# Kernel optimization log

Hardware: AMD Instinct MI355X
Metric: run time of the kernel (lower is better)

The kernel has to match this reference:

```python
import jax, jax.numpy as jnp
import numpy as np

D_MODEL = 2048
EXPAND = 2
D_INNER = D_MODEL * EXPAND            # 4096
HEAD_DIM = 64
NHEADS = D_INNER // HEAD_DIM          # 64
D_STATE = 128
NGROUPS = 1
D_CONV = 4
CHUNK = 256
CONV_DIM = D_INNER + 2 * NGROUPS * D_STATE      # 4352
D_IN_PROJ = 2 * D_INNER + 2 * NGROUPS * D_STATE + NHEADS  # 8512
EPS = 1e-5


def segsum(x):
    # x: [..., T] -> [..., T, T] lower-triangular segment sums (incl. diagonal)
    T = x.shape[-1]
    xc = jnp.cumsum(x, axis=-1)
    diff = xc[..., :, None] - xc[..., None, :]
    mask = jnp.tril(jnp.ones((T, T), dtype=bool))
    return jnp.where(mask, diff, -jnp.inf)


def causal_conv1d(x, w, b):
    # x: [B,L,C]  depthwise causal conv, kernel K; w: [C,K], b: [C]
    K = w.shape[1]
    L = x.shape[1]
    xp = jnp.pad(x, ((0, 0), (K - 1, 0), (0, 0)))
    y = b[None, None, :]
    for k in range(K):
        y = y + xp[:, k:k + L, :] * w[None, None, :, k]
    return jax.nn.silu(y)


def ssd_chunked(x, dt, A, B, C, Dskip):
    # x:[b,l,h,p] dt:[b,l,h] A:[h] B,C:[b,l,g,n] Dskip:[h]
    b, l, h, p = x.shape
    g, n = B.shape[2], B.shape[3]
    c = l // CHUNK
    xc = x.reshape(b, c, CHUNK, h, p)
    dtc = dt.reshape(b, c, CHUNK, h)
    Bh = jnp.repeat(B.reshape(b, c, CHUNK, g, n), h // g, axis=3)  # [b,c,s,h,n]
    Ch = jnp.repeat(C.reshape(b, c, CHUNK, g, n), h // g, axis=3)
    dA = dtc * A[None, None, None, :]            # [b,c,s,h]
    dAc = jnp.moveaxis(dA, 3, 1)                 # [b,h,c,s]
    A_cumsum = jnp.cumsum(dAc, axis=-1)          # [b,h,c,s]
    Lmat = jnp.exp(segsum(dAc))                  # [b,h,c,s,s]
    # intra-chunk (diagonal blocks)
    Y_diag = jnp.einsum('bclhn,bcshn,bhcls,bcsh,bcshp->bclhp', Ch, Bh, Lmat, dtc, xc)
    # per-chunk final states
    decay_states = jnp.exp(A_cumsum[..., -1:] - A_cumsum)   # [b,h,c,s]
    states = jnp.einsum('bclhn,bhcl,bclh,bclhp->bchpn', Bh, decay_states, dtc, xc)
    states = jnp.concatenate([jnp.zeros_like(states[:, :1]), states], axis=1)  # [b,c+1,h,p,n]
    # inter-chunk recurrence
    chunk_sums = jnp.pad(A_cumsum[..., -1], ((0, 0), (0, 0), (1, 0)))  # [b,h,c+1]
    decay_chunk = jnp.exp(segsum(chunk_sums))    # [b,h,c+1,c+1]
    new_states = jnp.einsum('bhzc,bchpn->bzhpn', decay_chunk, states)
    states_prev = new_states[:, :-1]             # state entering each chunk
    state_decay_out = jnp.exp(A_cumsum)          # [b,h,c,s]
    Y_off = jnp.einsum('bclhn,bchpn,bhcl->bclhp', Ch, states_prev, state_decay_out)
    Y = (Y_diag + Y_off).reshape(b, l, h, p) + x * Dskip[None, None, :, None]
    return Y


def gated_rmsnorm(y, z, w):
    # norm_before_gate=False: rmsnorm(y * silu(z)) * w, grouped (g=NGROUPS)
    x = y * jax.nn.silu(z)
    gs = D_INNER // NGROUPS
    xg = x.reshape(x.shape[:-1] + (NGROUPS, gs))
    var = jnp.mean(xg * xg, axis=-1, keepdims=True)
    xg = xg * jax.lax.rsqrt(var + EPS)
    return xg.reshape(x.shape) * w[None, None, :]


def setup_inputs() -> dict:
    key = jax.random.key(0)
    ks = jax.random.split(key, 9)
    B, L = 2, 2048
    return {
        'hidden_states': jax.random.normal(ks[0], (B, L, D_MODEL), jnp.float32),
        'W_in': jax.random.normal(ks[1], (D_MODEL, D_IN_PROJ), jnp.float32) * 0.02,
        'conv_w': jax.random.normal(ks[2], (CONV_DIM, D_CONV), jnp.float32) * 0.2,
        'conv_b': jax.random.normal(ks[3], (CONV_DIM,), jnp.float32) * 0.02,
        'A': -jnp.exp(jax.random.normal(ks[4], (NHEADS,), jnp.float32) * 0.5),
        'D': jax.random.normal(ks[5], (NHEADS,), jnp.float32) * 0.5,
        'dt_bias': jax.random.normal(ks[6], (NHEADS,), jnp.float32) * 0.5,
        'norm_w': jnp.ones((D_INNER,), jnp.float32) + jax.random.normal(ks[7], (D_INNER,), jnp.float32) * 0.02,
        'W_out': jax.random.normal(ks[8], (D_INNER, D_MODEL), jnp.float32) * 0.02,
    }


def reference(hidden_states, W_in, conv_w, conv_b, A, D, dt_bias, norm_w, W_out):
    b, l, _ = hidden_states.shape
    zxbcdt = hidden_states @ W_in  # [b,l,d_in_proj]
    z = zxbcdt[..., :D_INNER]
    xbc = zxbcdt[..., D_INNER:D_INNER + CONV_DIM]
    dt = zxbcdt[..., D_INNER + CONV_DIM:]
    xbc = causal_conv1d(xbc, conv_w, conv_b)
    x = xbc[..., :D_INNER].reshape(b, l, NHEADS, HEAD_DIM)
    Bs = xbc[..., D_INNER:D_INNER + NGROUPS * D_STATE].reshape(b, l, NGROUPS, D_STATE)
    Cs = xbc[..., D_INNER + NGROUPS * D_STATE:].reshape(b, l, NGROUPS, D_STATE)
    dt = jax.nn.softplus(dt + dt_bias[None, None, :])
    y = ssd_chunked(x, dt, A, Bs, Cs, D).reshape(b, l, D_INNER)
    y = gated_rmsnorm(y, z, norm_w)
    return y @ W_out
```

## Files before the change

kernel.cpp:

```cpp
#include <hip/hip_runtime.h>
#include <hip/hip_bf16.h>
#include <math.h>

#define D_MODEL   2048
#define D_INNER   4096
#define NHEADS    64
#define HEAD_DIM  64
#define D_STATE   128
#define CHUNK     256
#define CONV_DIM  (D_INNER + 2*D_STATE)
#define D_IN_PROJ (2*D_INNER + 2*D_STATE + NHEADS)
#define LD_ZX     8704
#define DT_OFF    (2*D_INNER + 2*D_STATE)
#define BATCH     2
#define SEQ       2048
#define NCHUNK    (SEQ/CHUNK)
#define EPS_RMS   1e-5f
#define MROWS     4096
#define TSTRIDE   ((size_t)MROWS * 512)

typedef unsigned short u16;
typedef __attribute__((ext_vector_type(8))) unsigned short u16x8;
typedef __attribute__((ext_vector_type(4))) unsigned short u16x4;
typedef __attribute__((ext_vector_type(8))) short bf16x8;
typedef __attribute__((ext_vector_type(4))) float f32x4;

__device__ __forceinline__ float us2f(u16 u){
    union { unsigned int i; float f; } c; c.i = ((unsigned int)u) << 16; return c.f;
}
__device__ __forceinline__ u16 f2us(float f){
    union { float f; unsigned int i; } c; c.f = f;
    unsigned int r = c.i + 0x7FFFu + ((c.i >> 16) & 1u);
    return (u16)(r >> 16);
}
__device__ __forceinline__ float siluf(float x){ return x / (1.f + expf(-x)); }

__device__ __forceinline__ void gload_lds16(const void* g, void* l) {
    __builtin_amdgcn_global_load_lds((const __attribute__((address_space(1))) void*)g,
                                     (__attribute__((address_space(3))) void*)l, 16, 0, 0);
}

#define VMCNT(n) asm volatile("s_waitcnt vmcnt(" #n ")" ::: "memory")

__device__ __forceinline__ void stage_half(const u16* __restrict__ g, size_t ldk,
                                           u16* ldsbase, int w, int lane)
{
    #pragma unroll
    for (int cc = 0; cc < 2; cc++) {
        int cb = cc * 512 + w * 64;
        int ci = cb + lane;
        int sc = ci ^ ((ci >> 3) & 7);
        gload_lds16(&g[(size_t)(sc >> 3) * ldk + (sc & 7) * 8], ldsbase + cb * 8);
    }
}

__global__ __launch_bounds__(256)
void cvt_bf16(const float* __restrict__ in, u16* __restrict__ out, int n4)
{
    int i = blockIdx.x * 256 + threadIdx.x;
    if (i >= n4) return;
    float4 v = *(const float4*)&in[(size_t)i * 4];
    u16x4 o; o[0]=f2us(v.x); o[1]=f2us(v.y); o[2]=f2us(v.z); o[3]=f2us(v.w);
    *(u16x4*)&out[(size_t)i * 4] = o;
}

__global__ __launch_bounds__(256)
void add2_bf16(float* __restrict__ out, const u16* __restrict__ t0,
               const u16* __restrict__ t1, int n8)
{
    int i = blockIdx.x * 256 + threadIdx.x;
    if (i >= n8) return;
    u16x8 a = *(const u16x8*)&t0[(size_t)i * 8];
    u16x8 b = *(const u16x8*)&t1[(size_t)i * 8];
    float* o = &out[(size_t)i * 8];
    *(float4*)&o[0] = make_float4(us2f(a[0])+us2f(b[0]), us2f(a[1])+us2f(b[1]),
                                  us2f(a[2])+us2f(b[2]), us2f(a[3])+us2f(b[3]));
    *(float4*)&o[4] = make_float4(us2f(a[4])+us2f(b[4]), us2f(a[5])+us2f(b[5]),
                                  us2f(a[6])+us2f(b[6]), us2f(a[7])+us2f(b[7]));
}

__global__ __launch_bounds__(256)
void transpose_cvt(const float* __restrict__ in, u16* __restrict__ out, int K, int N)
{
    __shared__ u16 tile[64][65];
    int k0 = blockIdx.x * 64;
    int n0 = blockIdx.y * 64;
    int t = threadIdx.x;
    #pragma unroll
    for (int q = 0; q < 16; q++) {
        int lin = q * 256 + t;
        int r = lin >> 6, c = lin & 63;
        int n = n0 + c;
        float v = (n < N) ? in[(size_t)(k0 + r) * N + n] : 0.f;
        tile[r][c] = f2us(v);
    }
    __syncthreads();
    #pragma unroll
    for (int q = 0; q < 4; q++) {
        int lin = q * 256 + t;
        int r = lin >> 4, cg = lin & 15;
        u16x4 v;
        #pragma unroll
        for (int e = 0; e < 4; e++) v[e] = tile[cg*4 + e][r];
        *(u16x4*)&out[(size_t)(n0 + r) * K + k0 + cg*4] = v;
    }
}

template<typename TC, bool KSPLIT>
__global__ __launch_bounds__(512, 1)
void gemm_8ph(const u16* __restrict__ Ag, const u16* __restrict__ Btg,
              TC* __restrict__ Cg, u16* __restrict__ Cg2,
              int M, int N, int Kext, int ldk, int ldc)
{
    __shared__ u16 smA[2][2][8192];
    __shared__ u16 smB[2][2][8192];
    const int tid = threadIdx.x;
    const int lane = tid & 63, w = tid >> 6;
    const int wm = w >> 2, wn = w & 3;
    const int lr = lane & 15, kh = lane >> 4;
    const int swz = (lr & 7) << 3;

    int orig = blockIdx.x;
    int ntile = gridDim.x;
    int kidx = 0;
    if constexpr (KSPLIT) { kidx = orig & 1; orig >>= 1; ntile >>= 1; }

    const int nbx = N >> 8;
    const int qq = ntile >> 3, r8 = ntile & 7;
    const int xcd = orig & 7, loc = orig >> 3;
    const int wgid = (xcd < r8 ? xcd*(qq+1) : r8*(qq+1) + (xcd-r8)*qq) + loc;
    const int m0 = (wgid / nbx) * 256;
    const int n0 = (wgid % nbx) * 256;

    if constexpr (KSPLIT) {
        Ag  += (size_t)kidx * Kext;
        Btg += (size_t)kidx * Kext;
        Cg2 += (size_t)kidx * M * ldc;
    }
    const int NT = Kext >> 6;

    f32x4 acc[8][4];
    #pragma unroll
    for (int i = 0; i < 8; i++)
        #pragma unroll
        for (int j = 0; j < 4; j++) acc[i][j] = (f32x4){0.f,0.f,0.f,0.f};

    stage_half(&Ag [(size_t)(m0      ) * ldk      ], ldk, &smA[0][0][0], w, lane);
    stage_half(&Ag [(size_t)(m0 + 128) * ldk      ], ldk, &smA[0][1][0], w, lane);
    stage_half(&Btg[(size_t)(n0      ) * ldk      ], ldk, &smB[0][0][0], w, lane);
    stage_half(&Btg[(size_t)(n0 + 128) * ldk      ], ldk, &smB[0][1][0], w, lane);
    stage_half(&Ag [(size_t)(m0      ) * ldk + 64 ], ldk, &smA[1][0][0], w, lane);
    stage_half(&Btg[(size_t)(n0      ) * ldk + 64 ], ldk, &smB[1][0][0], w, lane);
    stage_half(&Btg[(size_t)(n0 + 128) * ldk + 64 ], ldk, &smB[1][1][0], w, lane);
    VMCNT(6);
    __builtin_amdgcn_s_barrier();

    for (int t = 0; t < NT; ++t) {
        const int d = t & 1;
        const u16* As = &smA[d][wm][0];
        const u16* Bs = &smB[d][wn >> 1][0];
        const int rb = (wn & 1) * 64;

        bf16x8 aF[4][2], bLo[2][2], bHi[2][2];

        #pragma unroll
        for (int i = 0; i < 4; i++)
            #pragma unroll
            for (int ks = 0; ks < 2; ks++)
                aF[i][ks] = *(const bf16x8*)&As[(i*16 + lr)*64 + ((ks*32 + kh*8) ^ swz)];
        #pragma unroll
        for (int j = 0; j < 2; j++)
            #pragma unroll
            for (int ks = 0; ks < 2; ks++)
                bLo[j][ks] = *(const bf16x8*)&Bs[(rb + j*16 + lr)*64 + ((ks*32 + kh*8) ^ swz)];
        if (t + 1 < NT)
            stage_half(&Ag[(size_t)(m0 + 128) * ldk + (t+1)*64], ldk, &smA[d^1][1][0], w, lane);
        __builtin_amdgcn_s_barrier();
        __builtin_amdgcn_s_setprio(1);
        #pragma unroll
        for (int i = 0; i < 4; i++)
            #pragma unroll
            for (int j = 0; j < 2; j++)
                #pragma unroll
                for (int ks = 0; ks < 2; ks++)
                    acc[i][j] = __builtin_amdgcn_mfma_f32_16x16x32_bf16(aF[i][ks], bLo[j][ks], acc[i][j], 0, 0, 0);
        __builtin_amdgcn_s_setprio(0);
        __builtin_amdgcn_s_barrier();

        #pragma unroll
        for (int j = 0; j < 2; j++)
            #pragma unroll
            for (int ks = 0; ks < 2; ks++)
                bHi[j][ks] = *(const bf16x8*)&Bs[(rb + (2+j)*16 + lr)*64 + ((ks*32 + kh*8) ^ swz)];
        __builtin_amdgcn_s_barrier();
        __builtin_amdgcn_s_setprio(1);
        #pragma unroll
        for (int i = 0; i < 4; i++)
            #pragma unroll
            for (int j = 0; j < 2; j++)
                #pragma unroll
                for (int ks = 0; ks < 2; ks++)
                    acc[i][2+j] = __builtin_amdgcn_mfma_f32_16x16x32_bf16(aF[i][ks], bHi[j][ks], acc[i][2+j], 0, 0, 0);
        __builtin_amdgcn_s_setprio(0);
        __builtin_amdgcn_s_barrier();

        #pragma unroll
        for (int i = 0; i < 4; i++)
            #pragma unroll
            for (int ks = 0; ks < 2; ks++)
                aF[i][ks] = *(const bf16x8*)&As[(64 + i*16 + lr)*64 + ((ks*32 + kh*8) ^ swz)];
        if (t + 2 < NT)
            stage_half(&Btg[(size_t)(n0) * ldk + (t+2)*64], ldk, &smB[d][0][0], w, lane);
        __builtin_amdgcn_s_barrier();
        __builtin_amdgcn_s_setprio(1);
        #pragma unroll
        for (int i = 0; i < 4; i++)
            #pragma unroll
            for (int j = 0; j < 2; j++)
                #pragma unroll
                for (int ks = 0; ks < 2; ks++)
                    acc[4+i][j] = __builtin_amdgcn_mfma_f32_16x16x32_bf16(aF[i][ks], bLo[j][ks], acc[4+i][j], 0, 0, 0);
        __builtin_amdgcn_s_setprio(0);
        __builtin_amdgcn_s_barrier();

        if (t + 2 < NT) {
            stage_half(&Btg[(size_t)(n0 + 128) * ldk + (t+2)*64], ldk, &smB[d][1][0], w, lane);
            stage_half(&Ag [(size_t)(m0      ) * ldk + (t+2)*64], ldk, &smA[d][0][0], w, lane);
        }
        __builtin_amdgcn_s_barrier();
        __builtin_amdgcn_s_setprio(1);
        #pragma unroll
        for (int i = 0; i < 4; i++)
            #pragma unroll
            for (int j = 0; j < 2; j++)
                #pragma unroll
                for (int ks = 0; ks < 2; ks++)
                    acc[4+i][2+j] = __builtin_amdgcn_mfma_f32_16x16x32_bf16(aF[i][ks], bHi[j][ks], acc[4+i][2+j], 0, 0, 0);
        __builtin_amdgcn_s_setprio(0);
        if (t < NT - 2)       { VMCNT(6); }
        else if (t == NT - 2) { VMCNT(0); }
        __builtin_amdgcn_s_barrier();
    }

    #pragma unroll
    for (int mf = 0; mf < 8; mf++) {
        #pragma unroll
        for (int nf = 0; nf < 4; nf++) {
            int r = m0 + wm*128 + mf*16 + kh*4;
            int cidx = n0 + wn*64 + nf*16 + lr;
            #pragma unroll
            for (int q = 0; q < 4; q++) {
                if constexpr (KSPLIT) {
                    Cg2[(size_t)(r+q)*ldc + cidx] = f2us(acc[mf][nf][q]);
                } else if constexpr (sizeof(TC) == 4) {
                    Cg[(size_t)(r+q)*ldc + cidx] = acc[mf][nf][q];
                } else {
                    Cg[(size_t)(r+q)*ldc + cidx] = f2us(acc[mf][nf][q]);
                }
            }
        }
    }
}

__global__ __launch_bounds__(256)
void gemm_tail_ks4(const u16* __restrict__ A, const u16* __restrict__ Bt,
                   float* __restrict__ Cp, int M, int ldk)
{
    __shared__ u16 Asm[128][32];
    __shared__ u16 Bsm[128][32];
    const int t = threadIdx.x;
    const int lane = t & 63, w = t >> 6;
    const int wr = w >> 1, wc = w & 1;
    const int lr = lane & 15, kh = lane >> 4;

    const int bid = blockIdx.x;
    const int kidx = bid & 3, tile = bid >> 2;
    const int m0 = (tile >> 2) * 128;
    const int n0 = (tile & 3) * 128;

    const u16* Ak = A  + kidx * 512;
    const u16* Bk = Bt + kidx * 512;
    float* C = Cp + (size_t)kidx * TSTRIDE;

    f32x4 acc[4][4];
    #pragma unroll
    for (int i = 0; i < 4; i++)
        #pragma unroll
        for (int j = 0; j < 4; j++) acc[i][j] = (f32x4){0.f,0.f,0.f,0.f};

    for (int k0 = 0; k0 < 512; k0 += 32) {
        #pragma unroll
        for (int i = 0; i < 2; i++) {
            int cb = i * 256 + w * 64;
            int chunk = cb + lane;
            int row = chunk >> 2, kb = chunk & 3;
            gload_lds16(&Ak[(size_t)(m0 + row) * ldk + k0 + kb * 8], &Asm[0][0] + cb * 8);
            gload_lds16(&Bk[(size_t)(n0 + row) * ldk + k0 + kb * 8], &Bsm[0][0] + cb * 8);
        }
        __syncthreads();
        bf16x8 af[4], bf[4];
        #pragma unroll
        for (int i = 0; i < 4; i++)
            af[i] = *(const bf16x8*)&Asm[wr*64 + i*16 + lr][kh*8];
        #pragma unroll
        for (int j = 0; j < 4; j++)
            bf[j] = *(const bf16x8*)&Bsm[wc*64 + j*16 + lr][kh*8];
        #pragma unroll
        for (int i = 0; i < 4; i++)
            #pragma unroll
            for (int j = 0; j < 4; j++)
                acc[i][j] = __builtin_amdgcn_mfma_f32_16x16x32_bf16(af[i], bf[j], acc[i][j], 0, 0, 0);
        __syncthreads();
    }
    #pragma unroll
    for (int i = 0; i < 4; i++) {
        #pragma unroll
        for (int j = 0; j < 4; j++) {
            int r = m0 + wr*64 + i*16 + kh*4;
            int cidx = n0 + wc*64 + j*16 + lr;
            #pragma unroll
            for (int q = 0; q < 4; q++)
                C[(size_t)(r+q)*512 + cidx] = acc[i][j][q];
        }
    }
}

__global__ __launch_bounds__(256)
void conv_silu(const u16* __restrict__ zx, const float* __restrict__ tailp,
               const float* __restrict__ cw, const float* __restrict__ cb,
               u16* __restrict__ xconv, u16* __restrict__ Bbuf, u16* __restrict__ Cbuf)
{
    int idx = blockIdx.x * 256 + threadIdx.x;
    int cg = idx % (CONV_DIM / 8);
    int r  = idx / (CONV_DIM / 8);
    int c0 = cg * 8;
    int l  = r & (SEQ - 1);

    float y[8];
    {
        float4 b0 = *(const float4*)&cb[c0];
        float4 b1 = *(const float4*)&cb[c0 + 4];
        y[0]=b0.x; y[1]=b0.y; y[2]=b0.z; y[3]=b0.w;
        y[4]=b1.x; y[5]=b1.y; y[6]=b1.z; y[7]=b1.w;
    }
    float cwf[8][4];
    #pragma unroll
    for (int e = 0; e < 8; e++) {
        float4 v = *(const float4*)&cw[(c0 + e) * 4];
        cwf[e][0]=v.x; cwf[e][1]=v.y; cwf[e][2]=v.z; cwf[e][3]=v.w;
    }
    if (c0 < D_INNER) {
        #pragma unroll
        for (int k = 0; k < 4; k++) {
            if (l + k - 3 >= 0) {
                u16x8 v = *(const u16x8*)&zx[(size_t)(r + k - 3) * LD_ZX + D_INNER + c0];
                #pragma unroll
                for (int e = 0; e < 8; e++) y[e] += us2f(v[e]) * cwf[e][k];
            }
        }
    } else {
        int tc = c0 - D_INNER;
        #pragma unroll
        for (int k = 0; k < 4; k++) {
            if (l + k - 3 >= 0) {
                const float* tb = &tailp[(size_t)(r + k - 3) * 512 + tc];
                #pragma unroll
                for (int e = 0; e < 8; e++) {
                    float s = tb[e] + tb[TSTRIDE + e] + tb[2*TSTRIDE + e] + tb[3*TSTRIDE + e];
                    y[e] += s * cwf[e][k];
                }
            }
        }
    }
    u16x8 o;
    #pragma unroll
    for (int e = 0; e < 8; e++) {
        float s = y[e] / (1.f + expf(-y[e]));
        o[e] = f2us(s);
    }
    if (c0 < D_INNER)                *(u16x8*)&xconv[(size_t)r * D_INNER + c0] = o;
    else if (c0 < D_INNER + D_STATE) *(u16x8*)&Bbuf[(size_t)r * D_STATE + (c0 - D_INNER)] = o;
    else                             *(u16x8*)&Cbuf[(size_t)r * D_STATE + (c0 - D_INNER - D_STATE)] = o;
}

__global__ __launch_bounds__(256)
void dt_acs(const float* __restrict__ tailp, const float* __restrict__ Aparam,
            const float* __restrict__ dt_bias, float* __restrict__ dtT,
            float* __restrict__ Acs)
{
    __shared__ float sb[CHUNK];
    int blk = blockIdx.x;
    int c = blk & 7, h = (blk >> 3) & 63, b = blk >> 9;
    int t = threadIdx.x;
    int lg = c * CHUNK + t;
    int row = b * SEQ + lg;
    const float* tb = &tailp[(size_t)row * 512 + 256 + h];
    float x = tb[0] + tb[TSTRIDE] + tb[2*TSTRIDE] + tb[3*TSTRIDE];
    x += dt_bias[h];
    float dt = (x > 20.f) ? x : log1pf(expf(x));
    float v = dt * Aparam[h];
    sb[t] = v; __syncthreads();
    #pragma unroll
    for (int off = 1; off < 256; off <<= 1) {
        float add = (t >= off) ? sb[t - off] : 0.f;
        __syncthreads();
        v += add; sb[t] = v;
        __syncthreads();
    }
    int o = (b * NHEADS + h) * SEQ + lg;
    dtT[o] = dt;
    Acs[o] = v;
}

__global__ __launch_bounds__(256)
void s_precompute(const u16* __restrict__ Bbuf, const u16* __restrict__ Cbuf,
                  u16* __restrict__ Sbuf)
{
    int p = blockIdx.x % 10, bc = blockIdx.x / 10;
    int q = (p >= 6) ? 3 : (p >= 3) ? 2 : (p >= 1) ? 1 : 0;
    int st = p - q * (q + 1) / 2;
    int b = bc >> 3, c = bc & 7;
    const int lane = threadIdx.x & 63, w = threadIdx.x >> 6;
    const int lr = lane & 15, kh = lane >> 4;
    const size_t rowbase = (size_t)(b * SEQ + c * CHUNK);

    f32x4 sacc[4];
    #pragma unroll
    for (int i = 0; i < 4; i++) sacc[i] = (f32x4){0.f,0.f,0.f,0.f};
    #pragma unroll
    for (int kk = 0; kk < 4; kk++) {
        bf16x8 bA = *(const bf16x8*)&Bbuf[(rowbase + st*64 + w*16 + lr) * D_STATE + kk*32 + kh*8];
        #pragma unroll
        for (int i = 0; i < 4; i++) {
            bf16x8 af = *(const bf16x8*)&Cbuf[(rowbase + q*64 + i*16 + lr) * D_STATE + kk*32 + kh*8];
            sacc[i] = __builtin_amdgcn_mfma_f32_16x16x32_bf16(bA, af, sacc[i], 0, 0, 0);
        }
    }
    u16* Sb = Sbuf + (size_t)bc * 256 * 256;
    #pragma unroll
    for (int i = 0; i < 4; i++) {
        u16x4 o;
        #pragma unroll
        for (int qq = 0; qq < 4; qq++) o[qq] = f2us(sacc[i][qq]);
        *(u16x4*)&Sb[(size_t)(q*64 + i*16 + lr) * 256 + st*64 + w*16 + kh*4] = o;
    }
}

__global__ __launch_bounds__(256)
void chunk_states_mfma(const u16* __restrict__ xconv, const u16* __restrict__ Bbuf,
                       const float* __restrict__ dtT, const float* __restrict__ Acs,
                       u16* __restrict__ states)
{
    __shared__ u16 Btsh[128][72];
    __shared__ u16 xtsh[64][72];
    __shared__ float acs_sh[CHUNK];
    __shared__ float dt_sh[CHUNK];

    const int blk = blockIdx.x;
    const int h = blk & 63, c = (blk >> 6) & 7, b = blk >> 9;
    const int t = threadIdx.x;
    const int lane = t & 63, w = t >> 6;
    const int wr = w >> 1, wc = w & 1;
    const int lr = lane & 15, kh = lane >> 4;
    const int bh = b * NHEADS + h;
    const size_t rowbase = (size_t)(b * SEQ + c * CHUNK);

    acs_sh[t] = Acs[(size_t)bh * SEQ + c * CHUNK + t];
    dt_sh[t]  = dtT[(size_t)bh * SEQ + c * CHUNK + t];
    __syncthreads();
    const float acs_last = acs_sh[CHUNK - 1];

    f32x4 acc[4][2];
    #pragma unroll
    for (int j = 0; j < 4; j++)
        #pragma unroll
        for (int i = 0; i < 2; i++) acc[j][i] = (f32x4){0.f,0.f,0.f,0.f};

    for (int lt = 0; lt < 4; lt++) {
        __syncthreads();
        const int s = t & 63;
        const int sg = lt * 64 + s;
        const float wgt = dt_sh[sg] * expf(acs_last - acs_sh[sg]);
        {
            int ng = (t >> 6) * 32;
            const u16* src = &Bbuf[(rowbase + sg) * D_STATE + ng];
            #pragma unroll
            for (int q = 0; q < 4; q++) {
                u16x8 v = *(const u16x8*)&src[q * 8];
                #pragma unroll
                for (int e = 0; e < 8; e++)
                    Btsh[ng + q*8 + e][s] = v[e];
            }
        }
        {
            int pg = (t >> 6) * 16;
            const u16* src = &xconv[(rowbase + sg) * D_INNER + h * HEAD_DIM + pg];
            u16x8 v0 = *(const u16x8*)&src[0];
            u16x8 v1 = *(const u16x8*)&src[8];
            #pragma unroll
            for (int e = 0; e < 8; e++) {
                xtsh[pg + e][s]     = f2us(us2f(v0[e]) * wgt);
                xtsh[pg + 8 + e][s] = f2us(us2f(v1[e]) * wgt);
            }
        }
        __syncthreads();
        #pragma unroll
        for (int kk = 0; kk < 2; kk++) {
            bf16x8 xf[2], bf[4];
            #pragma unroll
            for (int i = 0; i < 2; i++)
                xf[i] = *(const bf16x8*)&xtsh[wr*32 + i*16 + lr][kk*32 + kh*8];
            #pragma unroll
            for (int j = 0; j < 4; j++)
                bf[j] = *(const bf16x8*)&Btsh[wc*64 + j*16 + lr][kk*32 + kh*8];
            #pragma unroll
            for (int j = 0; j < 4; j++)
                #pragma unroll
                for (int i = 0; i < 2; i++)
                    acc[j][i] = __builtin_amdgcn_mfma_f32_16x16x32_bf16(bf[j], xf[i], acc[j][i], 0, 0, 0);
        }
    }
    size_t base = ((size_t)((b*NCHUNK + c)*NHEADS + h)) * (HEAD_DIM * D_STATE);
    #pragma unroll
    for (int j = 0; j < 4; j++) {
        #pragma unroll
        for (int i = 0; i < 2; i++) {
            int p = wr*32 + i*16 + lr;
            int n = wc*64 + j*16 + kh*4;
            u16x4 o;
            #pragma unroll
            for (int q = 0; q < 4; q++) o[q] = f2us(acc[j][i][q]);
            *(u16x4*)&states[base + (size_t)p * D_STATE + n] = o;
        }
    }
}

__global__ __launch_bounds__(256)
void state_recurrence(u16* __restrict__ states, const float* __restrict__ Acs)
{
    int idx = blockIdx.x * 256 + threadIdx.x;
    int n8 = idx & 15;
    int p  = (idx >> 4) & 63;
    int bh = idx >> 10;
    int b = bh >> 6, h = bh & 63;
    float E[8];
    #pragma unroll
    for (int e = 0; e < 8; e++) E[e] = 0.f;
    for (int c = 0; c < NCHUNK; c++) {
        size_t off = ((size_t)((b*NCHUNK + c)*NHEADS + h)) * 8192 + (size_t)p * 128 + n8 * 8;
        u16x8 sv = *(const u16x8*)&states[off];
        u16x8 ev;
        #pragma unroll
        for (int e = 0; e < 8; e++) ev[e] = f2us(E[e]);
        *(u16x8*)&states[off] = ev;
        float g = expf(Acs[(size_t)(b*NHEADS + h) * SEQ + c*CHUNK + 255]);
        #pragma unroll
        for (int e = 0; e < 8; e++) E[e] = g * E[e] + us2f(sv[e]);
    }
}

__global__ __launch_bounds__(256, 1)
void chunk_output_mfma(const u16* __restrict__ xconv, const u16* __restrict__ Sbuf,
                       const u16* __restrict__ Cbuf, const float* __restrict__ dtT,
                       const float* __restrict__ Acs, const u16* __restrict__ states,
                       const float* __restrict__ Dparam, u16* __restrict__ Y)
{
    __shared__ u16 Bsm[64][136];
    __shared__ u16 xt[64][72];
    __shared__ u16 Pt[4][64][72];
    __shared__ float acs_sh[CHUNK];
    __shared__ float dt_sh[CHUNK];

    const int blk = blockIdx.x;
    const int h = blk & 63, c = (blk >> 6) & 7, b = blk >> 9;
    const int t = threadIdx.x;
    const int lane = t & 63, w = t >> 6;
    const int lr = lane & 15, kh = lane >> 4;
    const int bh = b * NHEADS + h;
    const size_t rowbase = (size_t)(b * SEQ + c * CHUNK);
    const u16* Sblk = Sbuf + (size_t)(b * NCHUNK + c) * 256 * 256;

    acs_sh[t] = Acs[(size_t)bh * SEQ + c * CHUNK + t];
    dt_sh[t]  = dtT[(size_t)bh * SEQ + c * CHUNK + t];

    bf16x8 af[4][4];
    #pragma unroll
    for (int i = 0; i < 4; i++)
        #pragma unroll
        for (int kk = 0; kk < 4; kk++)
            af[i][kk] = *(const bf16x8*)&Cbuf[(rowbase + w*64 + i*16 + lr) * D_STATE + kk*32 + kh*8];

    {
        int p = t >> 2, ng = (t & 3) * 32;
        const u16* src = &states[((size_t)((b*NCHUNK + c)*NHEADS + h)) * 8192 + (size_t)p * 128 + ng];
        #pragma unroll
        for (int q = 0; q < 4; q++)
            *(u16x8*)&Bsm[p][ng + q*8] = *(const u16x8*)&src[q*8];
    }
    __syncthreads();
    float acs_l[4], el[4];
    #pragma unroll
    for (int i = 0; i < 4; i++) { acs_l[i] = acs_sh[w*64 + i*16 + lr]; el[i] = expf(acs_l[i]); }

    f32x4 yacc[4][4];
    #pragma unroll
    for (int j = 0; j < 4; j++)
        #pragma unroll
        for (int i = 0; i < 4; i++) yacc[j][i] = (f32x4){0.f,0.f,0.f,0.f};
    #pragma unroll
    for (int kk = 0; kk < 4; kk++) {
        bf16x8 pvA[4];
        #pragma unroll
        for (int j = 0; j < 4; j++)
            pvA[j] = *(const bf16x8*)&Bsm[j*16 + lr][kk*32 + kh*8];
        #pragma unroll
        for (int j = 0; j < 4; j++)
            #pragma unroll
            for (int i = 0; i < 4; i++)
                yacc[j][i] = __builtin_amdgcn_mfma_f32_16x16x32_bf16(pvA[j], af[i][kk], yacc[j][i], 0, 0, 0);
    }
    #pragma unroll
    for (int j = 0; j < 4; j++)
        #pragma unroll
        for (int i = 0; i < 4; i++)
            #pragma unroll
            for (int q = 0; q < 4; q++)
                yacc[j][i][q] *= el[i];

    for (int st = 0; st < 4; st++) {
        __syncthreads();
        {
            int s = t & 63, pg = t >> 6;
            const u16* src = &xconv[(rowbase + st*64 + s) * D_INNER + h*HEAD_DIM + pg*16];
            u16x8 v0 = *(const u16x8*)&src[0];
            u16x8 v1 = *(const u16x8*)&src[8];
            #pragma unroll
            for (int q = 0; q < 8; q++) { xt[pg*16 + q][s] = v0[q]; xt[pg*16 + 8 + q][s] = v1[q]; }
        }
        __syncthreads();
        if (st > w) continue;

        #pragma unroll
        for (int js = 0; js < 4; js++) {
            int s0 = st*64 + js*16;
            float as0 = acs_sh[s0];
            int sgq = s0 + kh*4;
            float eneg[4];
            #pragma unroll
            for (int q = 0; q < 4; q++)
                eneg[q] = expf(fminf(as0 - acs_sh[sgq + q], 60.f)) * dt_sh[sgq + q];
            #pragma unroll
            for (int i = 0; i < 4; i++) {
                int ll = w*64 + i*16 + lr;
                float eladj = expf(acs_l[i] - as0);
                u16x4 sv = *(const u16x4*)&Sblk[(size_t)ll * 256 + sgq];
                u16x4 pv;
                #pragma unroll
                for (int q = 0; q < 4; q++) {
                    float fac = (sgq + q <= ll) ? eladj * eneg[q] : 0.f;
                    pv[q] = f2us(us2f(sv[q]) * fac);
                }
                *(u16x4*)&Pt[w][i*16 + lr][js*16 + kh*4] = pv;
            }
        }
        #pragma unroll
        for (int kk2 = 0; kk2 < 2; kk2++) {
            bf16x8 xA[4], pB[4];
            #pragma unroll
            for (int j = 0; j < 4; j++)
                xA[j] = *(const bf16x8*)&xt[j*16 + lr][kk2*32 + kh*8];
            #pragma unroll
            for (int i = 0; i < 4; i++)
                pB[i] = *(const bf16x8*)&Pt[w][i*16 + lr][kk2*32 + kh*8];
            #pragma unroll
            for (int j = 0; j < 4; j++)
                #pragma unroll
                for (int i = 0; i < 4; i++)
                    yacc[j][i] = __builtin_amdgcn_mfma_f32_16x16x32_bf16(xA[j], pB[i], yacc[j][i], 0, 0, 0);
        }
    }

    float Dh = Dparam[h];
    #pragma unroll
    for (int i = 0; i < 4; i++) {
        #pragma unroll
        for (int j = 0; j < 4; j++) {
            size_t o = (rowbase + w*64 + i*16 + lr) * D_INNER + h*HEAD_DIM + j*16 + kh*4;
            u16x4 xv = *(const u16x4*)&xconv[o];
            u16x4 ov;
            #pragma unroll
            for (int q = 0; q < 4; q++)
                ov[q] = f2us(yacc[j][i][q] + Dh * us2f(xv[q]));
            *(u16x4*)&Y[o] = ov;
        }
    }
}

__global__ __launch_bounds__(256)
void gated_rmsnorm_k(u16* __restrict__ Y, const u16* __restrict__ zx,
                     const float* __restrict__ nw)
{
    __shared__ float xs[D_INNER];
    __shared__ float red[8];
    int row = blockIdx.x;
    int t = threadIdx.x;
    float ss = 0.f;
    for (int i = t*8; i < D_INNER; i += 2048) {
        u16x8 yv = *(const u16x8*)&Y[(size_t)row * D_INNER + i];
        u16x8 zv = *(const u16x8*)&zx[(size_t)row * LD_ZX + i];
        #pragma unroll
        for (int q = 0; q < 8; q++) {
            float x = us2f(yv[q]) * siluf(us2f(zv[q]));
            xs[i + q] = x;
            ss += x * x;
        }
    }
    #pragma unroll
    for (int off = 32; off > 0; off >>= 1) ss += __shfl_down(ss, off);
    int wid = t >> 6, lane = t & 63;
    if (lane == 0) red[wid] = ss;
    __syncthreads();
    if (t == 0) {
        float tot = red[0] + red[1] + red[2] + red[3];
        red[0] = rsqrtf(tot / (float)D_INNER + EPS_RMS);
    }
    __syncthreads();
    float sc = red[0];
    for (int i = t*8; i < D_INNER; i += 2048) {
        u16x8 o;
        #pragma unroll
        for (int q = 0; q < 8; q++) o[q] = f2us(xs[i + q] * sc * nw[i + q]);
        *(u16x8*)&Y[(size_t)row * D_INNER + i] = o;
    }
}

__global__ void ws_fail_k(float* out, float mb){ out[threadIdx.x] = mb; }

extern "C" void kernel_launch(void* const* d_in, const int* in_sizes, int n_in,
                              void* d_out, int out_size, void* d_ws, size_t ws_size,
                              hipStream_t stream)
{
    const float* hidden  = (const float*)d_in[0];
    const float* W_in    = (const float*)d_in[1];
    const float* conv_w  = (const float*)d_in[2];
    const float* conv_b  = (const float*)d_in[3];
    const float* Aparam  = (const float*)d_in[4];
    const float* Dparam  = (const float*)d_in[5];
    const float* dt_bias = (const float*)d_in[6];
    const float* norm_w  = (const float*)d_in[7];
    const float* W_out   = (const float*)d_in[8];
    float* out = (float*)d_out;

    const int M = BATCH * SEQ;

    size_t off = 0;
    char* wsb = (char*)d_ws;
    u16*   zx     = (u16*)  (wsb + off); off += (size_t)M * LD_ZX * 2;
    u16*   xconv  = (u16*)  (wsb + off); off += (size_t)M * D_INNER * 2;
    u16*   Bbuf   = (u16*)  (wsb + off); off += (size_t)M * D_STATE * 2;
    u16*   Cbuf   = (u16*)  (wsb + off); off += (size_t)M * D_STATE * 2;
    float* dtT    = (float*)(wsb + off); off += (size_t)BATCH * NHEADS * SEQ * 4;
    float* Acs    = (float*)(wsb + off); off += (size_t)BATCH * NHEADS * SEQ * 4;
    u16*   states = (u16*)  (wsb + off); off += (size_t)BATCH * NCHUNK * NHEADS * HEAD_DIM * D_STATE * 2;
    u16*   Ybuf   = (u16*)  (wsb + off); off += (size_t)M * D_INNER * 2;
    u16*   hbf    = (u16*)  (wsb + off); off += (size_t)M * D_MODEL * 2;
    u16*   WtIn   = (u16*)  (wsb + off); off += (size_t)LD_ZX * D_MODEL * 2;
    u16*   WtOut  = (u16*)  (wsb + off); off += (size_t)D_MODEL * D_INNER * 2;
    float* tailp  = (float*)(wsb + off); off += 4 * TSTRIDE * 4;
    u16*   Sbuf   = (u16*)  (wsb + off); off += (size_t)16 * 256 * 256 * 2;
    u16*   tmpf   = (u16*)zx;

    if (off > ws_size) {
        ws_fail_k<<<1, 64, 0, stream>>>(out, (float)(ws_size >> 20));
        return;
    }

    cvt_bf16<<<(M * D_MODEL / 4 + 255) / 256, 256, 0, stream>>>(hidden, hbf, M * D_MODEL / 4);
    transpose_cvt<<<dim3(D_MODEL/64, LD_ZX/64), 256, 0, stream>>>(W_in, WtIn, D_MODEL, D_IN_PROJ);
    transpose_cvt<<<dim3(D_INNER/64, D_MODEL/64), 256, 0, stream>>>(W_out, WtOut, D_INNER, D_MODEL);

    gemm_8ph<u16, false><<<(8192/256) * (M/256), 512, 0, stream>>>(
        hbf, WtIn, zx, nullptr, M, 8192, D_MODEL, D_MODEL, LD_ZX);
    gemm_tail_ks4<<<512, 256, 0, stream>>>(hbf, WtIn + (size_t)8192 * D_MODEL, tailp, M, D_MODEL);

    conv_silu<<<(M * CONV_DIM / 8) / 256, 256, 0, stream>>>(zx, tailp, conv_w, conv_b, xconv, Bbuf, Cbuf);
    s_precompute<<<160, 256, 0, stream>>>(Bbuf, Cbuf, Sbuf);
    dt_acs<<<BATCH * NHEADS * NCHUNK, 256, 0, stream>>>(tailp, Aparam, dt_bias, dtT, Acs);
    chunk_states_mfma<<<BATCH * NCHUNK * NHEADS, 256, 0, stream>>>(xconv, Bbuf, dtT, Acs, states);
    state_recurrence<<<(BATCH * NHEADS * 64 * 16) / 256, 256, 0, stream>>>(states, Acs);
    chunk_output_mfma<<<BATCH * NCHUNK * NHEADS, 256, 0, stream>>>(xconv, Sbuf, Cbuf, dtT, Acs, states, Dparam, Ybuf);
    gated_rmsnorm_k<<<M, 256, 0, stream>>>(Ybuf, zx, norm_w);

    gemm_8ph<float, true><<<2 * (D_MODEL/256) * (M/256), 512, 0, stream>>>(
        Ybuf, WtOut, out, tmpf, M, D_MODEL, D_INNER/2, D_INNER, D_MODEL);
    add2_bf16<<<(M * D_MODEL / 8 + 255) / 256, 256, 0, stream>>>(
        out, tmpf, tmpf + (size_t)M * D_MODEL, M * D_MODEL / 8);
}
```

Before: 466.9 us.

## Merge prep and mid kernels; pre-transpose B once per chunk for states

Combines the hidden-state conversion and both weight transposes into one launch, and merges S precompute and dt/cumsum into one launch that also writes a pre-transposed copy of B per chunk. chunk_states_mfma then loads the transposed B with vector copies instead of doing a scattered per-element transpose into shared memory in every one of its 1024 blocks. chunk_output_mfma aliases its prev-state buffer onto the P tile buffer to shrink shared memory and raise occupancy. This saves launches and redundant transposes, at the cost of an extra BT buffer and the BT-writing blocks sharing a launch with uneven work.

```diff
diff --git a/kernel.cpp b/kernel.cpp
--- a/kernel.cpp
+++ b/kernel.cpp
@@ -11,7 +11,6 @@
 #define CONV_DIM  (D_INNER + 2*D_STATE)
 #define D_IN_PROJ (2*D_INNER + 2*D_STATE + NHEADS)
 #define LD_ZX     8704
-#define DT_OFF    (2*D_INNER + 2*D_STATE)
 #define BATCH     2
 #define SEQ       2048
 #define NCHUNK    (SEQ/CHUNK)
@@ -55,13 +54,48 @@
 }
 
 __global__ __launch_bounds__(256)
-void cvt_bf16(const float* __restrict__ in, u16* __restrict__ out, int n4)
-{
-    int i = blockIdx.x * 256 + threadIdx.x;
-    if (i >= n4) return;
-    float4 v = *(const float4*)&in[(size_t)i * 4];
-    u16x4 o; o[0]=f2us(v.x); o[1]=f2us(v.y); o[2]=f2us(v.z); o[3]=f2us(v.w);
-    *(u16x4*)&out[(size_t)i * 4] = o;
+void prep_kernel(const float* __restrict__ hidden, u16* __restrict__ hbf,
+                 const float* __restrict__ W_in, u16* __restrict__ WtIn,
+                 const float* __restrict__ W_out, u16* __restrict__ WtOut)
+{
+    __shared__ u16 tile[64][65];
+    int bid = blockIdx.x;
+    int t = threadIdx.x;
+    if (bid < 8192) {
+        int i = bid * 256 + t;
+        float4 v = *(const float4*)&hidden[(size_t)i * 4];
+        u16x4 o; o[0]=f2us(v.x); o[1]=f2us(v.y); o[2]=f2us(v.z); o[3]=f2us(v.w);
+        *(u16x4*)&hbf[(size_t)i * 4] = o;
+        return;
+    }
+    const float* in; u16* out; int K, N, k0, n0;
+    if (bid < 8192 + 4352) {
+        int b2 = bid - 8192;
+        in = W_in; out = WtIn; K = D_MODEL; N = D_IN_PROJ;
+        k0 = (b2 % 32) * 64; n0 = (b2 / 32) * 64;
+    } else {
+        int b3 = bid - 8192 - 4352;
+        in = W_out; out = WtOut; K = D_INNER; N = D_MODEL;
+        k0 = (b3 % 64) * 64; n0 = (b3 / 64) * 64;
+    }
+    #pragma unroll
+    for (int q = 0; q < 16; q++) {
+        int lin = q * 256 + t;
+        int r = lin >> 6, c = lin & 63;
+        int n = n0 + c;
+        float v = (n < N) ? in[(size_t)(k0 + r) * N + n] : 0.f;
+        tile[r][c] = f2us(v);
+    }
+    __syncthreads();
+    #pragma unroll
+    for (int q = 0; q < 4; q++) {
+        int lin = q * 256 + t;
+        int r = lin >> 4, cg = lin & 15;
+        u16x4 v;
+        #pragma unroll
+        for (int e = 0; e < 4; e++) v[e] = tile[cg*4 + e][r];
+        *(u16x4*)&out[(size_t)(n0 + r) * K + k0 + cg*4] = v;
+    }
 }
 
 __global__ __launch_bounds__(256)
@@ -79,33 +113,6 @@
                                   us2f(a[6])+us2f(b[6]), us2f(a[7])+us2f(b[7]));
 }
 
-__global__ __launch_bounds__(256)
-void transpose_cvt(const float* __restrict__ in, u16* __restrict__ out, int K, int N)
-{
-    __shared__ u16 tile[64][65];
-    int k0 = blockIdx.x * 64;
-    int n0 = blockIdx.y * 64;
-    int t = threadIdx.x;
-    #pragma unroll
-    for (int q = 0; q < 16; q++) {
-        int lin = q * 256 + t;
-        int r = lin >> 6, c = lin & 63;
-        int n = n0 + c;
-        float v = (n < N) ? in[(size_t)(k0 + r) * N + n] : 0.f;
-        tile[r][c] = f2us(v);
-    }
-    __syncthreads();
-    #pragma unroll
-    for (int q = 0; q < 4; q++) {
-        int lin = q * 256 + t;
-        int r = lin >> 4, cg = lin & 15;
-        u16x4 v;
-        #pragma unroll
-        for (int e = 0; e < 4; e++) v[e] = tile[cg*4 + e][r];
-        *(u16x4*)&out[(size_t)(n0 + r) * K + k0 + cg*4] = v;
-    }
-}
-
 template<typename TC, bool KSPLIT>
 __global__ __launch_bounds__(512, 1)
 void gemm_8ph(const u16* __restrict__ Ag, const u16* __restrict__ Btg,
@@ -384,70 +391,100 @@
 }
 
 __global__ __launch_bounds__(256)
-void dt_acs(const float* __restrict__ tailp, const float* __restrict__ Aparam,
-            const float* __restrict__ dt_bias, float* __restrict__ dtT,
-            float* __restrict__ Acs)
-{
+void combo_mid(const u16* __restrict__ Bbuf, const u16* __restrict__ Cbuf,
+               u16* __restrict__ BT, u16* __restrict__ Sbuf,
+               const float* __restrict__ tailp, const float* __restrict__ Aparam,
+               const float* __restrict__ dt_bias, float* __restrict__ dtT,
+               float* __restrict__ Acs)
+{
+    __shared__ u16 tile[64][72];
     __shared__ float sb[CHUNK];
-    int blk = blockIdx.x;
-    int c = blk & 7, h = (blk >> 3) & 63, b = blk >> 9;
-    int t = threadIdx.x;
-    int lg = c * CHUNK + t;
-    int row = b * SEQ + lg;
-    const float* tb = &tailp[(size_t)row * 512 + 256 + h];
-    float x = tb[0] + tb[TSTRIDE] + tb[2*TSTRIDE] + tb[3*TSTRIDE];
-    x += dt_bias[h];
-    float dt = (x > 20.f) ? x : log1pf(expf(x));
-    float v = dt * Aparam[h];
-    sb[t] = v; __syncthreads();
-    #pragma unroll
-    for (int off = 1; off < 256; off <<= 1) {
-        float add = (t >= off) ? sb[t - off] : 0.f;
-        __syncthreads();
-        v += add; sb[t] = v;
-        __syncthreads();
-    }
-    int o = (b * NHEADS + h) * SEQ + lg;
-    dtT[o] = dt;
-    Acs[o] = v;
+    const int bid = blockIdx.x;
+    const int t = threadIdx.x;
+
+    if (bid < 16) {
+        int b = bid >> 3, c = bid & 7;
+        const size_t rowbase = (size_t)(b * SEQ + c * CHUNK);
+        u16* BTb = BT + (size_t)bid * 128 * 256;
+        for (int sub = 0; sub < 8; sub++) {
+            int l0 = (sub >> 1) * 64, n0 = (sub & 1) * 64;
+            #pragma unroll
+            for (int q = 0; q < 2; q++) {
+                int lin = q * 256 + t;
+                int r = lin >> 3, cc = (lin & 7) * 8;
+                *(u16x8*)&tile[r][cc] = *(const u16x8*)&Bbuf[(rowbase + l0 + r) * D_STATE + n0 + cc];
+            }
+            __syncthreads();
+            #pragma unroll
+            for (int q = 0; q < 4; q++) {
+                int lin = q * 256 + t;
+                int rn = lin >> 4, cg = lin & 15;
+                u16x4 v;
+                #pragma unroll
+                for (int e = 0; e < 4; e++) v[e] = tile[cg*4 + e][rn];
+                *(u16x4*)&BTb[(size_t)(n0 + rn) * 256 + l0 + cg*4] = v;
+            }
+            __syncthreads();
+        }
+        return;
+    }
+    if (bid < 176) {
+        int p = (bid - 16) % 10, bc = (bid - 16) / 10;
+        int q = (p >= 6) ? 3 : (p >= 3) ? 2 : (p >= 1) ? 1 : 0;
+        int st = p - q * (q + 1) / 2;
+        int b = bc >> 3, c = bc & 7;
+        const int lane = t & 63, w = t >> 6;
+        const int lr = lane & 15, kh = lane >> 4;
+        const size_t rowbase = (size_t)(b * SEQ + c * CHUNK);
+
+        f32x4 sacc[4];
+        #pragma unroll
+        for (int i = 0; i < 4; i++) sacc[i] = (f32x4){0.f,0.f,0.f,0.f};
+        #pragma unroll
+        for (int kk = 0; kk < 4; kk++) {
+            bf16x8 bA = *(const bf16x8*)&Bbuf[(rowbase + st*64 + w*16 + lr) * D_STATE + kk*32 + kh*8];
+            #pragma unroll
+            for (int i = 0; i < 4; i++) {
+                bf16x8 af = *(const bf16x8*)&Cbuf[(rowbase + q*64 + i*16 + lr) * D_STATE + kk*32 + kh*8];
+                sacc[i] = __builtin_amdgcn_mfma_f32_16x16x32_bf16(bA, af, sacc[i], 0, 0, 0);
+            }
+        }
+        u16* Sb = Sbuf + (size_t)bc * 256 * 256;
+        #pragma unroll
+        for (int i = 0; i < 4; i++) {
+            u16x4 o;
+            #pragma unroll
+            for (int qq = 0; qq < 4; qq++) o[qq] = f2us(sacc[i][qq]);
+            *(u16x4*)&Sb[(size_t)(q*64 + i*16 + lr) * 256 + st*64 + w*16 + kh*4] = o;
+        }
+        return;
+    }
+    {
+        int blk = bid - 176;
+        int c = blk & 7, h = (blk >> 3) & 63, b = blk >> 9;
+        int lg = c * CHUNK + t;
+        int row = b * SEQ + lg;
+        const float* tb = &tailp[(size_t)row * 512 + 256 + h];
+        float x = tb[0] + tb[TSTRIDE] + tb[2*TSTRIDE] + tb[3*TSTRIDE];
+        x += dt_bias[h];
+        float dt = (x > 20.f) ? x : log1pf(expf(x));
+        float v = dt * Aparam[h];
+        sb[t] = v; __syncthreads();
+        #pragma unroll
+        for (int off = 1; off < 256; off <<= 1) {
+            float add = (t >= off) ? sb[t - off] : 0.f;
+            __syncthreads();
+            v += add; sb[t] = v;
+            __syncthreads();
+        }
+        int o = (b * NHEADS + h) * SEQ + lg;
+        dtT[o] = dt;
+        Acs[o] = v;
+    }
 }
 
 __global__ __launch_bounds__(256)
-void s_precompute(const u16* __restrict__ Bbuf, const u16* __restrict__ Cbuf,
-                  u16* __restrict__ Sbuf)
-{
-    int p = blockIdx.x % 10, bc = blockIdx.x / 10;
-    int q = (p >= 6) ? 3 : (p >= 3) ? 2 : (p >= 1) ? 1 : 0;
-    int st = p - q * (q + 1) / 2;
-    int b = bc >> 3, c = bc & 7;
-    const int lane = threadIdx.x & 63, w = threadIdx.x >> 6;
-    const int lr = lane & 15, kh = lane >> 4;
-    const size_t rowbase = (size_t)(b * SEQ + c * CHUNK);
-
-    f32x4 sacc[4];
-    #pragma unroll
-    for (int i = 0; i < 4; i++) sacc[i] = (f32x4){0.f,0.f,0.f,0.f};
-    #pragma unroll
-    for (int kk = 0; kk < 4; kk++) {
-        bf16x8 bA = *(const bf16x8*)&Bbuf[(rowbase + st*64 + w*16 + lr) * D_STATE + kk*32 + kh*8];
-        #pragma unroll
-        for (int i = 0; i < 4; i++) {
-            bf16x8 af = *(const bf16x8*)&Cbuf[(rowbase + q*64 + i*16 + lr) * D_STATE + kk*32 + kh*8];
-            sacc[i] = __builtin_amdgcn_mfma_f32_16x16x32_bf16(bA, af, sacc[i], 0, 0, 0);
-        }
-    }
-    u16* Sb = Sbuf + (size_t)bc * 256 * 256;
-    #pragma unroll
-    for (int i = 0; i < 4; i++) {
-        u16x4 o;
-        #pragma unroll
-        for (int qq = 0; qq < 4; qq++) o[qq] = f2us(sacc[i][qq]);
-        *(u16x4*)&Sb[(size_t)(q*64 + i*16 + lr) * 256 + st*64 + w*16 + kh*4] = o;
-    }
-}
-
-__global__ __launch_bounds__(256)
-void chunk_states_mfma(const u16* __restrict__ xconv, const u16* __restrict__ Bbuf,
+void chunk_states_mfma(const u16* __restrict__ xconv, const u16* __restrict__ BT,
                        const float* __restrict__ dtT, const float* __restrict__ Acs,
                        u16* __restrict__ states)
 {
@@ -463,7 +500,9 @@
     const int wr = w >> 1, wc = w & 1;
     const int lr = lane & 15, kh = lane >> 4;
     const int bh = b * NHEADS + h;
+    const int bc = b * NCHUNK + c;
     const size_t rowbase = (size_t)(b * SEQ + c * CHUNK);
+    const u16* BTb = BT + (size_t)bc * 128 * 256;
 
     acs_sh[t] = Acs[(size_t)bh * SEQ + c * CHUNK + t];
     dt_sh[t]  = dtT[(size_t)bh * SEQ + c * CHUNK + t];
@@ -478,21 +517,17 @@
 
     for (int lt = 0; lt < 4; lt++) {
         __syncthreads();
-        const int s = t & 63;
-        const int sg = lt * 64 + s;
-        const float wgt = dt_sh[sg] * expf(acs_last - acs_sh[sg]);
         {
-            int ng = (t >> 6) * 32;
-            const u16* src = &Bbuf[(rowbase + sg) * D_STATE + ng];
-            #pragma unroll
-            for (int q = 0; q < 4; q++) {
-                u16x8 v = *(const u16x8*)&src[q * 8];
-                #pragma unroll
-                for (int e = 0; e < 8; e++)
-                    Btsh[ng + q*8 + e][s] = v[e];
-            }
+            int n = t >> 1, lc = (t & 1) * 32;
+            const u16* src = &BTb[(size_t)n * 256 + lt*64 + lc];
+            #pragma unroll
+            for (int q = 0; q < 4; q++)
+                *(u16x8*)&Btsh[n][lc + q*8] = *(const u16x8*)&src[q*8];
         }
         {
+            const int s = t & 63;
+            const int sg = lt * 64 + s;
+            const float wgt = dt_sh[sg] * expf(acs_last - acs_sh[sg]);
             int pg = (t >> 6) * 16;
             const u16* src = &xconv[(rowbase + sg) * D_INNER + h * HEAD_DIM + pg];
             u16x8 v0 = *(const u16x8*)&src[0];
@@ -520,7 +555,7 @@
                     acc[j][i] = __builtin_amdgcn_mfma_f32_16x16x32_bf16(bf[j], xf[i], acc[j][i], 0, 0, 0);
         }
     }
-    size_t base = ((size_t)((b*NCHUNK + c)*NHEADS + h)) * (HEAD_DIM * D_STATE);
+    size_t base = ((size_t)(bc * NHEADS + h)) * (HEAD_DIM * D_STATE);
     #pragma unroll
     for (int j = 0; j < 4; j++) {
         #pragma unroll
@@ -565,11 +600,11 @@
                        const float* __restrict__ Acs, const u16* __restrict__ states,
                        const float* __restrict__ Dparam, u16* __restrict__ Y)
 {
-    __shared__ u16 Bsm[64][136];
+    __shared__ u16 PtU[4][64][72];
     __shared__ u16 xt[64][72];
-    __shared__ u16 Pt[4][64][72];
     __shared__ float acs_sh[CHUNK];
     __shared__ float dt_sh[CHUNK];
+    u16 (*prevS)[136] = (u16(*)[136])&PtU[0][0][0];
 
     const int blk = blockIdx.x;
     const int h = blk & 63, c = (blk >> 6) & 7, b = blk >> 9;
@@ -595,7 +630,7 @@
         const u16* src = &states[((size_t)((b*NCHUNK + c)*NHEADS + h)) * 8192 + (size_t)p * 128 + ng];
         #pragma unroll
         for (int q = 0; q < 4; q++)
-            *(u16x8*)&Bsm[p][ng + q*8] = *(const u16x8*)&src[q*8];
+            *(u16x8*)&prevS[p][ng + q*8] = *(const u16x8*)&src[q*8];
     }
     __syncthreads();
     float acs_l[4], el[4];
@@ -612,7 +647,7 @@
         bf16x8 pvA[4];
         #pragma unroll
         for (int j = 0; j < 4; j++)
-            pvA[j] = *(const bf16x8*)&Bsm[j*16 + lr][kk*32 + kh*8];
+            pvA[j] = *(const bf16x8*)&prevS[j*16 + lr][kk*32 + kh*8];
         #pragma unroll
         for (int j = 0; j < 4; j++)
             #pragma unroll
@@ -660,7 +695,7 @@
                     float fac = (sgq + q <= ll) ? eladj * eneg[q] : 0.f;
                     pv[q] = f2us(us2f(sv[q]) * fac);
                 }
-                *(u16x4*)&Pt[w][i*16 + lr][js*16 + kh*4] = pv;
+                *(u16x4*)&PtU[w][i*16 + lr][js*16 + kh*4] = pv;
             }
         }
         #pragma unroll
@@ -671,7 +706,7 @@
                 xA[j] = *(const bf16x8*)&xt[j*16 + lr][kk2*32 + kh*8];
             #pragma unroll
             for (int i = 0; i < 4; i++)
-                pB[i] = *(const bf16x8*)&Pt[w][i*16 + lr][kk2*32 + kh*8];
+                pB[i] = *(const bf16x8*)&PtU[w][i*16 + lr][kk2*32 + kh*8];
             #pragma unroll
             for (int j = 0; j < 4; j++)
                 #pragma unroll
@@ -768,6 +803,7 @@
     u16*   WtOut  = (u16*)  (wsb + off); off += (size_t)D_MODEL * D_INNER * 2;
     float* tailp  = (float*)(wsb + off); off += 4 * TSTRIDE * 4;
     u16*   Sbuf   = (u16*)  (wsb + off); off += (size_t)16 * 256 * 256 * 2;
+    u16*   BT     = (u16*)  (wsb + off); off += (size_t)16 * 128 * 256 * 2;
     u16*   tmpf   = (u16*)zx;
 
     if (off > ws_size) {
@@ -775,18 +811,16 @@
         return;
     }
 
-    cvt_bf16<<<(M * D_MODEL / 4 + 255) / 256, 256, 0, stream>>>(hidden, hbf, M * D_MODEL / 4);
-    transpose_cvt<<<dim3(D_MODEL/64, LD_ZX/64), 256, 0, stream>>>(W_in, WtIn, D_MODEL, D_IN_PROJ);
-    transpose_cvt<<<dim3(D_INNER/64, D_MODEL/64), 256, 0, stream>>>(W_out, WtOut, D_INNER, D_MODEL);
+    prep_kernel<<<8192 + 4352 + 2048, 256, 0, stream>>>(hidden, hbf, W_in, WtIn, W_out, WtOut);
 
     gemm_8ph<u16, false><<<(8192/256) * (M/256), 512, 0, stream>>>(
         hbf, WtIn, zx, nullptr, M, 8192, D_MODEL, D_MODEL, LD_ZX);
     gemm_tail_ks4<<<512, 256, 0, stream>>>(hbf, WtIn + (size_t)8192 * D_MODEL, tailp, M, D_MODEL);
 
     conv_silu<<<(M * CONV_DIM / 8) / 256, 256, 0, stream>>>(zx, tailp, conv_w, conv_b, xconv, Bbuf, Cbuf);
-    s_precompute<<<160, 256, 0, stream>>>(Bbuf, Cbuf, Sbuf);
-    dt_acs<<<BATCH * NHEADS * NCHUNK, 256, 0, stream>>>(tailp, Aparam, dt_bias, dtT, Acs);
-    chunk_states_mfma<<<BATCH * NCHUNK * NHEADS, 256, 0, stream>>>(xconv, Bbuf, dtT, Acs, states);
+    combo_mid<<<16 + 160 + BATCH * NHEADS * NCHUNK, 256, 0, stream>>>(
+        Bbuf, Cbuf, BT, Sbuf, tailp, Aparam, dt_bias, dtT, Acs);
+    chunk_states_mfma<<<BATCH * NCHUNK * NHEADS, 256, 0, stream>>>(xconv, BT, dtT, Acs, states);
     state_recurrence<<<(BATCH * NHEADS * 64 * 16) / 256, 256, 0, stream>>>(states, Acs);
     chunk_output_mfma<<<BATCH * NCHUNK * NHEADS, 256, 0, stream>>>(xconv, Sbuf, Cbuf, dtT, Acs, states, Dparam, Ybuf);
     gated_rmsnorm_k<<<M, 256, 0, stream>>>(Ybuf, zx, norm_w);
```

New measurement: 472.4 us. No clear change (+1.2%).
